# Performance work log

Hardware: AMD Instinct MI355X
Metric: run time of the kernel (lower is better)

Reference implementation:

```python
import jax, jax.numpy as jnp
import numpy as np

V = 10000        # one-hot depth per sparse feature
N_DENSE = 13
N_SPARSE = 26
FIELD = N_DENSE + N_SPARSE       # 39
K = 8
FEAT = N_DENSE + N_SPARSE * V    # 260013
BATCH = 4096


def setup_inputs() -> dict:
    key = jax.random.key(0)
    k1, k2, k3, k4 = jax.random.split(key, 4)
    dense = jax.random.normal(k1, (BATCH, N_DENSE), dtype=jnp.float32)
    sparse = jax.random.randint(k2, (BATCH, N_SPARSE), 0, V)
    w0 = jnp.zeros((1,), dtype=jnp.float32)
    w = jax.random.normal(k3, (FEAT, 1), dtype=jnp.float32) * 0.05
    v = jax.random.normal(k4, (FEAT, FIELD, K), dtype=jnp.float32) * 0.05
    return {"dense": dense, "sparse": sparse, "w0": w0, "w": w, "v": v}


def reference(dense, sparse, w0, w, v):
    # Row offsets of each sparse feature's one-hot block inside the
    # concatenated feature vector x = [dense(13) | onehot_0(V) | ... | onehot_25(V)].
    offsets = N_DENSE + jnp.arange(N_SPARSE) * V          # [26]
    idx = sparse.astype(jnp.int32) + offsets[None, :]     # [B, 26] flat feature ids

    # linear_part = x @ w + w0  (one-hot matmul == gather)
    linear = dense @ w[:N_DENSE] \
        + jnp.sum(w[idx, 0], axis=1, keepdims=True) + w0  # [B, 1]

    # field_f = tensordot(x, v, axes=1): dense contribution + gathered rows
    field_f = jnp.einsum('bd,dfk->bfk', dense, v[:N_DENSE]) \
        + jnp.sum(v[idx], axis=1)                         # [B, FIELD, K]

    # sum_{i<j} <f_i, f_j> = 0.5 * (||sum_i f_i||^2 - sum_i ||f_i||^2)
    S = jnp.sum(field_f, axis=1)                          # [B, K]
    inter = 0.5 * (jnp.sum(S * S, axis=1)
                   - jnp.sum(field_f * field_f, axis=(1, 2)))  # [B]

    return linear + inter[:, None]                        # [B, 1]
```

## Files before the change

### kernel.cpp

```cpp
#include <hip/hip_runtime.h>


constexpr int V_DEPTH  = 10000;
constexpr int N_DENSE  = 13;
constexpr int N_SPARSE = 26;
constexpr int FIELD    = 39;
constexpr int K        = 8;
constexpr int FK       = FIELD * K;
constexpr int BLOCK    = 320;
constexpr int NWAVES   = BLOCK / 64;

__global__ __launch_bounds__(BLOCK) void ffm_fwd_kernel(
    const float* __restrict__ dense,
    const int*   __restrict__ sparse,
    const float* __restrict__ w0,
    const float* __restrict__ w,
    const float* __restrict__ v,
    float*       __restrict__ out)
{
    const int b = blockIdx.x;
    const int t = threadIdx.x;

    __shared__ float s_dense[N_DENSE];
    __shared__ int   s_idx[N_SPARSE];
    __shared__ float s_wg[N_SPARSE];
    __shared__ float s_sq[NWAVES];
    __shared__ float s_Sk[NWAVES][K];

    if (t < N_DENSE) s_dense[t] = dense[b * N_DENSE + t];
    if (t < N_SPARSE) {
        const int id = sparse[b * N_SPARSE + t] + N_DENSE + t * V_DEPTH;
        s_idx[t] = id;
        s_wg[t]  = w[id];
    }
    __syncthreads();

    float acc = 0.0f;
    if (t < FK) {
        #pragma unroll
        for (int d = 0; d < N_DENSE; ++d)
            acc += s_dense[d] * v[d * FK + t];
        #pragma unroll
        for (int j = 0; j < N_SPARSE; ++j)
            acc += v[(size_t)s_idx[j] * FK + t];
    }

    float sq = acc * acc;
    float sk = acc;
    #pragma unroll
    for (int off = 32; off >= 1; off >>= 1)
        sq += __shfl_xor(sq, off, 64);
    #pragma unroll
    for (int off = 32; off >= 8; off >>= 1)
        sk += __shfl_xor(sk, off, 64);

    const int wave = t >> 6;
    const int lane = t & 63;
    if (lane == 0) s_sq[wave] = sq;
    if (lane < K)  s_Sk[wave][lane] = sk;
    __syncthreads();

    if (t == 0) {
        float sumsq = 0.0f;
        #pragma unroll
        for (int wv = 0; wv < NWAVES; ++wv) sumsq += s_sq[wv];

        float ssum = 0.0f;
        #pragma unroll
        for (int k = 0; k < K; ++k) {
            float Sk = 0.0f;
            #pragma unroll
            for (int wv = 0; wv < NWAVES; ++wv) Sk += s_Sk[wv][k];
            ssum += Sk * Sk;
        }

        float linear = w0[0];
        #pragma unroll
        for (int j = 0; j < N_SPARSE; ++j) linear += s_wg[j];
        #pragma unroll
        for (int d = 0; d < N_DENSE; ++d)  linear += s_dense[d] * w[d];

        out[b] = linear + 0.5f * (ssum - sumsq);
    }
}

extern "C" void kernel_launch(void* const* d_in, const int* in_sizes, int n_in,
                              void* d_out, int out_size, void* d_ws, size_t ws_size,
                              hipStream_t stream) {
    const float* dense  = (const float*)d_in[0];
    const int*   sparse = (const int*)  d_in[1];
    const float* w0     = (const float*)d_in[2];
    const float* w      = (const float*)d_in[3];
    const float* v      = (const float*)d_in[4];
    float* out = (float*)d_out;

    const int batch = out_size;
    ffm_fwd_kernel<<<batch, BLOCK, 0, stream>>>(dense, sparse, w0, w, v, out);
}
```

Baseline: 389.6 us.

## Process four batch rows per block with float4 gathers and LDS reduction

Measured after the change: 390.4 us. No clear change (+0.2%).

```diff
diff --git a/kernel.cpp b/kernel.cpp
--- a/kernel.cpp
+++ b/kernel.cpp
@@ -7,8 +7,10 @@
 constexpr int FIELD    = 39;
 constexpr int K        = 8;
 constexpr int FK       = FIELD * K;
-constexpr int BLOCK    = 320;
-constexpr int NWAVES   = BLOCK / 64;
+constexpr int NV4      = 78;
+constexpr int TPR      = 80;
+constexpr int ROWS     = 4;
+constexpr int BLOCK    = TPR * ROWS;
 
 __global__ __launch_bounds__(BLOCK) void ffm_fwd_kernel(
     const float* __restrict__ dense,
@@ -18,69 +20,72 @@
     const float* __restrict__ v,
     float*       __restrict__ out)
 {
-    const int b = blockIdx.x;
-    const int t = threadIdx.x;
+    const int t   = threadIdx.x;
+    const int r   = t / TPR;
+    const int e   = t - r * TPR;
+    const int row = blockIdx.x * ROWS + r;
 
-    __shared__ float s_dense[N_DENSE];
-    __shared__ int   s_idx[N_SPARSE];
-    __shared__ float s_wg[N_SPARSE];
-    __shared__ float s_sq[NWAVES];
-    __shared__ float s_Sk[NWAVES][K];
+    __shared__ float  s_dense[ROWS][N_DENSE];
+    __shared__ int    s_idx[ROWS][N_SPARSE];
+    __shared__ float  s_wg[ROWS][N_SPARSE];
+    __shared__ float4 s_acc[ROWS][TPR];
+    __shared__ float  s_S[ROWS][K];
+    __shared__ float  s_Q[ROWS][K];
 
-    if (t < N_DENSE) s_dense[t] = dense[b * N_DENSE + t];
-    if (t < N_SPARSE) {
-        const int id = sparse[b * N_SPARSE + t] + N_DENSE + t * V_DEPTH;
-        s_idx[t] = id;
-        s_wg[t]  = w[id];
+    if (e < N_SPARSE) {
+        const int id = sparse[row * N_SPARSE + e] + N_DENSE + e * V_DEPTH;
+        s_idx[r][e] = id;
+        s_wg[r][e]  = w[id];
+    }
+    if (e >= 32 && e < 32 + N_DENSE)
+        s_dense[r][e - 32] = dense[row * N_DENSE + (e - 32)];
+    __syncthreads();
+
+    float4 acc = make_float4(0.f, 0.f, 0.f, 0.f);
+    if (e < NV4) {
+        #pragma unroll
+        for (int j = 0; j < N_SPARSE; ++j) {
+            const float4* p = (const float4*)(v + (size_t)s_idx[r][j] * FK);
+            const float4  x = p[e];
+            acc.x += x.x; acc.y += x.y; acc.z += x.z; acc.w += x.w;
+        }
+        #pragma unroll
+        for (int d = 0; d < N_DENSE; ++d) {
+            const float4* p = (const float4*)(v + d * FK);
+            const float4  x = p[e];
+            const float   s = s_dense[r][d];
+            acc.x += s * x.x; acc.y += s * x.y; acc.z += s * x.z; acc.w += s * x.w;
+        }
+    }
+    s_acc[r][e] = acc;
+    __syncthreads();
+
+    if (t < ROWS * K) {
+        const int rr = t >> 3, k = t & 7, g = k >> 2, c = k & 3;
+        float S = 0.f, Q = 0.f;
+        #pragma unroll
+        for (int f = 0; f < FIELD; ++f) {
+            const float a = ((const float*)&s_acc[rr][2 * f + g])[c];
+            S += a; Q += a * a;
+        }
+        s_S[rr][k] = S;
+        s_Q[rr][k] = Q;
     }
     __syncthreads();
 
-    float acc = 0.0f;
-    if (t < FK) {
-        #pragma unroll
-        for (int d = 0; d < N_DENSE; ++d)
-            acc += s_dense[d] * v[d * FK + t];
-        #pragma unroll
-        for (int j = 0; j < N_SPARSE; ++j)
-            acc += v[(size_t)s_idx[j] * FK + t];
-    }
-
-    float sq = acc * acc;
-    float sk = acc;
-    #pragma unroll
-    for (int off = 32; off >= 1; off >>= 1)
-        sq += __shfl_xor(sq, off, 64);
-    #pragma unroll
-    for (int off = 32; off >= 8; off >>= 1)
-        sk += __shfl_xor(sk, off, 64);
-
-    const int wave = t >> 6;
-    const int lane = t & 63;
-    if (lane == 0) s_sq[wave] = sq;
-    if (lane < K)  s_Sk[wave][lane] = sk;
-    __syncthreads();
-
-    if (t == 0) {
-        float sumsq = 0.0f;
-        #pragma unroll
-        for (int wv = 0; wv < NWAVES; ++wv) sumsq += s_sq[wv];
-
-        float ssum = 0.0f;
+    if (e == 0) {
+        float ssum = 0.f, sumsq = 0.f;
         #pragma unroll
         for (int k = 0; k < K; ++k) {
-            float Sk = 0.0f;
-            #pragma unroll
-            for (int wv = 0; wv < NWAVES; ++wv) Sk += s_Sk[wv][k];
-            ssum += Sk * Sk;
+            ssum  += s_S[r][k] * s_S[r][k];
+            sumsq += s_Q[r][k];
         }
-
-        float linear = w0[0];
+        float lin = w0[0];
         #pragma unroll
-        for (int j = 0; j < N_SPARSE; ++j) linear += s_wg[j];
+        for (int j = 0; j < N_SPARSE; ++j) lin += s_wg[r][j];
         #pragma unroll
-        for (int d = 0; d < N_DENSE; ++d)  linear += s_dense[d] * w[d];
-
-        out[b] = linear + 0.5f * (ssum - sumsq);
+        for (int d = 0; d < N_DENSE; ++d)  lin += s_dense[r][d] * w[d];
+        out[row] = lin + 0.5f * (ssum - sumsq);
     }
 }
 
@@ -95,5 +100,5 @@
     float* out = (float*)d_out;
 
     const int batch = out_size;
-    ffm_fwd_kernel<<<batch, BLOCK, 0, stream>>>(dense, sparse, w0, w, v, out);
+    ffm_fwd_kernel<<<batch / ROWS, BLOCK, 0, stream>>>(dense, sparse, w0, w, v, out);
 }
```
